# Kernel tuning notes

Measured on AMD Instinct MI355X. Metric: run time of the kernel, lower is better.

## Reference

```python
import jax, jax.numpy as jnp
import numpy as np

NUM_CLASSES = 91
BBOX_XFORM_CLIP = float(np.log(1000.0 / 16.0))
WX, WY, WW, WH = 10.0, 10.0, 5.0, 5.0  # torchvision BoxCoder weights
DETECTIONS_PER_IMG = 100


def _decode_boxes(reg, props):
    # reg: [P, 4*C], props: [P, 4] -> [P, C, 4]  (torchvision BoxCoder.decode)
    widths = props[:, 2] - props[:, 0]
    heights = props[:, 3] - props[:, 1]
    ctr_x = props[:, 0] + 0.5 * widths
    ctr_y = props[:, 1] + 0.5 * heights
    r = reg.reshape(reg.shape[0], -1, 4)
    dx = r[..., 0] / WX
    dy = r[..., 1] / WY
    dw = jnp.minimum(r[..., 2] / WW, BBOX_XFORM_CLIP)
    dh = jnp.minimum(r[..., 3] / WH, BBOX_XFORM_CLIP)
    pcx = dx * widths[:, None] + ctr_x[:, None]
    pcy = dy * heights[:, None] + ctr_y[:, None]
    pw = jnp.exp(dw) * widths[:, None]
    ph = jnp.exp(dh) * heights[:, None]
    return jnp.stack([pcx - 0.5 * pw, pcy - 0.5 * ph, pcx + 0.5 * pw, pcy + 0.5 * ph], axis=-1)


def _clip_boxes(boxes, h, w):
    x = jnp.clip(boxes[..., 0::2], 0.0, float(w))
    y = jnp.clip(boxes[..., 1::2], 0.0, float(h))
    return jnp.stack([x[..., 0], y[..., 0], x[..., 1], y[..., 1]], axis=-1)


def setup_inputs() -> dict:
    key = jax.random.key(0)
    k1, k2, k3, k4, k5 = jax.random.split(key, 5)
    B, P, C, FD = 8, 4096, NUM_CLASSES, 1024
    N = B * P
    class_logits = jax.random.normal(k1, (N, C), dtype=jnp.float32)
    box_regression = 0.5 * jax.random.normal(k2, (N, 4 * C), dtype=jnp.float32)
    # valid proposal boxes inside an 800x800 image: x1<x2, y1<y2
    xy = jax.random.uniform(k3, (N, 2), dtype=jnp.float32) * 700.0
    wh = jax.random.uniform(k4, (N, 2), dtype=jnp.float32) * 96.0 + 4.0
    proposals = jnp.concatenate([xy, xy + wh], axis=-1)
    box_features = jax.random.normal(k5, (N, FD), dtype=jnp.float32)
    return {"class_logits": class_logits, "box_regression": box_regression,
            "proposals": proposals, "box_features": box_features,
            "batch_size": B, "image_h": 800, "image_w": 800}


def reference(class_logits, box_regression, proposals, box_features, batch_size, image_h, image_w):
    B = int(batch_size)
    N = class_logits.shape[0]
    P = N // B
    lg = class_logits.reshape(B, P, NUM_CLASSES)
    rg = box_regression.reshape(B, P, 4 * NUM_CLASSES)
    pr = proposals.reshape(B, P, 4)
    ft = box_features.reshape(B, P, -1)

    def per_image(lg_i, rg_i, pr_i, ft_i):
        boxes = _decode_boxes(rg_i, pr_i)            # [P, C, 4]
        scores = jax.nn.softmax(lg_i, axis=-1)       # [P, C]
        boxes = _clip_boxes(boxes, image_h, image_w)
        boxes = boxes[:, 1:].reshape(-1, 4)          # drop background class -> [P*(C-1), 4]
        scores = scores[:, 1:].reshape(-1)
        # batched_nms with iou_threshold=1.0 never suppresses anything (IoU<=1 always),
        # so keep == indices sorted by score descending, truncated to detections_per_img.
        keep = jnp.argsort(-scores)[:DETECTIONS_PER_IMG]
        boxes = boxes / float(image_h)               # source divides by image_shape[0] only
        kept_boxes = boxes[keep]                     # [D, 4]
        feat_idx = keep // (NUM_CLASSES - 1)         # source: keep / (num_classes-1) int div
        kept_feats = ft_i[feat_idx]                  # [D, FD]
        return kept_boxes, kept_feats

    all_boxes, all_features = jax.vmap(per_image)(lg, rg, pr, ft)
    return all_boxes, all_features
```

## Files before the change

kernel.cpp:

```cpp
#include <hip/hip_runtime.h>
#include <hip/hip_bf16.h>

#define NCLS 91
#define NFG 90
#define NDET 100
#define FDIM 1024
#define CAP 4096
#define NBUK 4096
#define BBOX_CLIP 4.135166556742356f
#define K1_TPB 256
#define RPB 32
#define K2_TPB 1024

__global__ __launch_bounds__(K1_TPB) void k1_softhist(
        const float* __restrict__ logits, float* __restrict__ rowoff,
        unsigned* __restrict__ maxk, unsigned* __restrict__ ghist,
        int P, int bpi) {
    __shared__ unsigned hist[NBUK];
    for (int b = threadIdx.x; b < NBUK; b += K1_TPB) hist[b] = 0u;
    __syncthreads();
    int img = blockIdx.x / bpi;
    int blk = blockIdx.x % bpi;
    int wave = threadIdx.x >> 6, lane = threadIdx.x & 63;
    for (int it = 0; it < RPB / 4; it++) {
        int rl = blk * RPB + wave * (RPB / 4) + it;
        if (rl >= P) break;
        long long row = (long long)img * P + rl;
        const float* r = logits + row * NCLS;
        float l1 = r[lane];
        float l2 = (lane < NCLS - 64) ? r[64 + lane] : -INFINITY;
        float m = fmaxf(l1, l2);
        #pragma unroll
        for (int o = 32; o; o >>= 1) m = fmaxf(m, __shfl_xor(m, o));
        float e = expf(l1 - m) + ((lane < NCLS - 64) ? expf(l2 - m) : 0.0f);
        #pragma unroll
        for (int o = 32; o; o >>= 1) e += __shfl_xor(e, o);
        float off = m + logf(e);
        unsigned ka = (lane >= 1) ? __float_as_uint(expf(l1 - off)) : 0u;
        unsigned kb = (lane < NCLS - 64) ? __float_as_uint(expf(l2 - off)) : 0u;
        if (lane >= 1)        atomicAdd(&hist[ka >> 20], 1u);
        if (lane < NCLS - 64) atomicAdd(&hist[kb >> 20], 1u);
        unsigned km = ka > kb ? ka : kb;
        #pragma unroll
        for (int o = 32; o; o >>= 1) { unsigned t = __shfl_xor(km, o); km = km > t ? km : t; }
        if (lane == 0) { rowoff[row] = off; maxk[row] = km; }
    }
    __syncthreads();
    unsigned* gh = ghist + (size_t)img * NBUK;
    for (int b = threadIdx.x; b < NBUK; b += K1_TPB) {
        unsigned c = hist[b];
        if (c) atomicAdd(&gh[b], c);
    }
}

__global__ __launch_bounds__(K2_TPB) void k2_select(
        const float* __restrict__ logits, const float* __restrict__ reg,
        const float* __restrict__ props, const float* __restrict__ feats,
        const int* __restrict__ pH, const int* __restrict__ pW,
        const float* __restrict__ rowoff, const unsigned* __restrict__ maxk,
        const unsigned* __restrict__ ghist,
        float* __restrict__ outBoxes, float* __restrict__ outFeats, int P) {
    __shared__ unsigned long long cand[CAP];
    __shared__ unsigned hot[CAP];
    __shared__ unsigned tpart[256];
    __shared__ unsigned tsuf[257];
    __shared__ unsigned keepR[NDET];
    __shared__ unsigned sh_lb, sh_nhot, sh_ncand, sh_base;

    const int img = blockIdx.x;
    const int tid = threadIdx.x;
    const unsigned* gh = ghist + (size_t)img * NBUK;

    if (tid == 0) { sh_nhot = 0; sh_ncand = 0; sh_lb = 0; }

    unsigned local[16];
    if (tid < 256) {
        unsigned mn = 0xFFFFFFFFu;
        #pragma unroll
        for (int i = 0; i < 16; i++) { local[i] = gh[tid * 16 + i]; mn = mn < local[i] ? mn : local[i]; }
        tpart[tid] = mn;
    }
    __syncthreads();
    if (tid == 0) {
        unsigned mn = 0xFFFFFFFFu;
        for (int t = 0; t < 256; t++) mn = mn < tpart[t] ? mn : tpart[t];
        sh_base = mn;
    }
    __syncthreads();
    unsigned base = sh_base;

    if (tid < 256) {
        unsigned s = 0;
        #pragma unroll
        for (int i = 0; i < 16; i++) { local[i] -= base; s += local[i]; }
        tpart[tid] = s;
    }
    __syncthreads();
    if (tid == 0) {
        unsigned run = 0; tsuf[256] = 0;
        for (int t = 255; t >= 0; t--) { run += tpart[t]; tsuf[t] = run; }
    }
    __syncthreads();
    if (tid < 256) {
        unsigned run = tsuf[tid + 1];
        #pragma unroll
        for (int i = 15; i >= 0; i--) {
            unsigned prev = run; run += local[i];
            if (run >= NDET && prev < NDET) sh_lb = ((unsigned)(tid * 16 + i)) << 20;
        }
    }
    __syncthreads();
    const unsigned lb = sh_lb;

    const unsigned* mk = maxk + (size_t)img * P;
    for (int r = tid; r < P; r += K2_TPB)
        if (mk[r] >= lb) hot[atomicAdd(&sh_nhot, 1u)] = (unsigned)r;
    __syncthreads();
    const int nhot = (int)sh_nhot;

    const int wave = tid >> 6, lane = tid & 63;
    for (int i = wave; i < nhot; i += K2_TPB / 64) {
        int rl = (int)hot[i];
        long long row = (long long)img * P + rl;
        float off = rowoff[row];
        const float* r = logits + row * NCLS;
        float l1 = r[lane];
        float l2 = (lane < NCLS - 64) ? r[64 + lane] : -INFINITY;
        if (lane >= 1) {
            unsigned k = __float_as_uint(expf(l1 - off));
            if (k >= lb) {
                unsigned pos = atomicAdd(&sh_ncand, 1u);
                if (pos < CAP)
                    cand[pos] = ((unsigned long long)k << 32) |
                                (unsigned)(0xFFFFFFFFu - (unsigned)(rl * NFG + lane - 1));
            }
        }
        if (lane < NCLS - 64) {
            unsigned k = __float_as_uint(expf(l2 - off));
            if (k >= lb) {
                unsigned pos = atomicAdd(&sh_ncand, 1u);
                if (pos < CAP)
                    cand[pos] = ((unsigned long long)k << 32) |
                                (unsigned)(0xFFFFFFFFu - (unsigned)(rl * NFG + 63 + lane));
            }
        }
    }
    __syncthreads();
    unsigned cnt = sh_ncand; if (cnt > CAP) cnt = CAP;

    int n = 128; while (n < (int)cnt) n <<= 1;
    for (int i = tid; i < n; i += K2_TPB) if (i >= (int)cnt) cand[i] = 0ULL;
    __syncthreads();
    for (int k = 2; k <= n; k <<= 1) {
        for (int j = k >> 1; j > 0; j >>= 1) {
            for (int i = tid; i < n; i += K2_TPB) {
                int ixj = i ^ j;
                if (ixj > i) {
                    bool up = ((i & k) == 0);
                    unsigned long long a = cand[i], b = cand[ixj];
                    if ((a > b) == up) { cand[i] = b; cand[ixj] = a; }
                }
            }
            __syncthreads();
        }
    }

    if (tid < NDET) {
        unsigned long long key = cand[n - 1 - tid];
        unsigned e = 0xFFFFFFFFu - (unsigned)(key & 0xFFFFFFFFull);
        int pr = e / NFG, cm = e - pr * NFG, c = cm + 1;
        long long rw = (long long)img * P + pr;
        float x1 = props[rw * 4 + 0], y1 = props[rw * 4 + 1];
        float x2 = props[rw * 4 + 2], y2 = props[rw * 4 + 3];
        float w = x2 - x1, hgt = y2 - y1;
        float cx = x1 + 0.5f * w, cy = y1 + 0.5f * hgt;
        const float* rr = reg + rw * (4 * NCLS) + 4 * c;
        float dx = rr[0] / 10.0f, dy = rr[1] / 10.0f;
        float dw = fminf(rr[2] / 5.0f, BBOX_CLIP);
        float dh = fminf(rr[3] / 5.0f, BBOX_CLIP);
        float pcx = dx * w + cx, pcy = dy * hgt + cy;
        float pw_ = expf(dw) * w, ph_ = expf(dh) * hgt;
        float bx1 = pcx - 0.5f * pw_, by1 = pcy - 0.5f * ph_;
        float bx2 = pcx + 0.5f * pw_, by2 = pcy + 0.5f * ph_;
        float W = (float)(*pW), H = (float)(*pH);
        bx1 = fminf(fmaxf(bx1, 0.0f), W);
        bx2 = fminf(fmaxf(bx2, 0.0f), W);
        by1 = fminf(fmaxf(by1, 0.0f), H);
        by2 = fminf(fmaxf(by2, 0.0f), H);
        int o = (img * NDET + tid) * 4;
        outBoxes[o + 0] = bx1 / H;
        outBoxes[o + 1] = by1 / H;
        outBoxes[o + 2] = bx2 / H;
        outBoxes[o + 3] = by2 / H;
        keepR[tid] = (unsigned)rw;
    }
    __syncthreads();

    int g = tid >> 8, l = tid & 255;
    for (int r0 = 0; r0 < (NDET + 3) / 4; r0++) {
        int d = r0 * 4 + g;
        if (d < NDET) {
            long long rw = keepR[d];
            const float4* src = (const float4*)(feats + rw * FDIM);
            float4* dst = (float4*)(outFeats + ((long long)img * NDET + d) * FDIM);
            dst[l] = src[l];
        }
    }
}

extern "C" void kernel_launch(void* const* d_in, const int* in_sizes, int n_in,
                              void* d_out, int out_size, void* d_ws, size_t ws_size,
                              hipStream_t stream) {
    const float* logits = (const float*)d_in[0];
    const float* reg    = (const float*)d_in[1];
    const float* props  = (const float*)d_in[2];
    const float* feats  = (const float*)d_in[3];
    const int*   pH     = (const int*)d_in[5];
    const int*   pW     = (const int*)d_in[6];

    int N = in_sizes[0] / NCLS;
    int B = out_size / (NDET * (4 + FDIM));
    int P = N / B;
    int bpi = (P + RPB - 1) / RPB;

    char* ws = (char*)d_ws;
    float*    rowoff = (float*)ws;
    unsigned* maxk   = (unsigned*)(rowoff + N);
    unsigned* ghist  = (unsigned*)(maxk + N);

    float* outBoxes = (float*)d_out;
    float* outFeats = outBoxes + (size_t)B * NDET * 4;

    k1_softhist<<<B * bpi, K1_TPB, 0, stream>>>(logits, rowoff, maxk, ghist, P, bpi);
    k2_select<<<B, K2_TPB, 0, stream>>>(logits, reg, props, feats, pH, pW,
                                        rowoff, maxk, ghist, outBoxes, outFeats, P);
}
```

Measured before the change: 242.0 us.

## Build per-image histogram from row max keys and split feature gather into kernel

The first kernel no longer builds a per-score shared histogram or does global atomics. It only computes each row's log-sum-exp offset and maximum score key. The selection kernel now builds a histogram of the per-row maxima (P entries) in shared memory to find the threshold bucket, which removes the per-class atomics and the global histogram. The feature copy moves out of the 8-block selection kernel into a separate kernel with one block per detection, so it runs across many CUs. The trade-off is an extra launch and a coarser threshold from row maxima, which may admit more hot rows.

```diff
diff --git a/kernel.cpp b/kernel.cpp
--- a/kernel.cpp
+++ b/kernel.cpp
@@ -7,25 +7,20 @@
 #define FDIM 1024
 #define CAP 4096
 #define NBUK 4096
+#define PMAX 4096
 #define BBOX_CLIP 4.135166556742356f
 #define K1_TPB 256
 #define RPB 32
 #define K2_TPB 1024
 
-__global__ __launch_bounds__(K1_TPB) void k1_softhist(
+__global__ __launch_bounds__(K1_TPB) void k1_soft(
         const float* __restrict__ logits, float* __restrict__ rowoff,
-        unsigned* __restrict__ maxk, unsigned* __restrict__ ghist,
-        int P, int bpi) {
-    __shared__ unsigned hist[NBUK];
-    for (int b = threadIdx.x; b < NBUK; b += K1_TPB) hist[b] = 0u;
-    __syncthreads();
-    int img = blockIdx.x / bpi;
-    int blk = blockIdx.x % bpi;
+        unsigned* __restrict__ maxk, int N) {
     int wave = threadIdx.x >> 6, lane = threadIdx.x & 63;
+    int rowbase = blockIdx.x * RPB + wave * (RPB / 4);
     for (int it = 0; it < RPB / 4; it++) {
-        int rl = blk * RPB + wave * (RPB / 4) + it;
-        if (rl >= P) break;
-        long long row = (long long)img * P + rl;
+        long long row = rowbase + it;
+        if (row >= N) return;
         const float* r = logits + row * NCLS;
         float l1 = r[lane];
         float l2 = (lane < NCLS - 64) ? r[64 + lane] : -INFINITY;
@@ -38,61 +33,43 @@
         float off = m + logf(e);
         unsigned ka = (lane >= 1) ? __float_as_uint(expf(l1 - off)) : 0u;
         unsigned kb = (lane < NCLS - 64) ? __float_as_uint(expf(l2 - off)) : 0u;
-        if (lane >= 1)        atomicAdd(&hist[ka >> 20], 1u);
-        if (lane < NCLS - 64) atomicAdd(&hist[kb >> 20], 1u);
         unsigned km = ka > kb ? ka : kb;
         #pragma unroll
         for (int o = 32; o; o >>= 1) { unsigned t = __shfl_xor(km, o); km = km > t ? km : t; }
         if (lane == 0) { rowoff[row] = off; maxk[row] = km; }
     }
-    __syncthreads();
-    unsigned* gh = ghist + (size_t)img * NBUK;
-    for (int b = threadIdx.x; b < NBUK; b += K1_TPB) {
-        unsigned c = hist[b];
-        if (c) atomicAdd(&gh[b], c);
-    }
 }
 
 __global__ __launch_bounds__(K2_TPB) void k2_select(
         const float* __restrict__ logits, const float* __restrict__ reg,
-        const float* __restrict__ props, const float* __restrict__ feats,
+        const float* __restrict__ props,
         const int* __restrict__ pH, const int* __restrict__ pW,
         const float* __restrict__ rowoff, const unsigned* __restrict__ maxk,
-        const unsigned* __restrict__ ghist,
-        float* __restrict__ outBoxes, float* __restrict__ outFeats, int P) {
+        float* __restrict__ outBoxes, unsigned* __restrict__ keepRow, int P) {
     __shared__ unsigned long long cand[CAP];
-    __shared__ unsigned hot[CAP];
+    __shared__ unsigned hist[NBUK];
+    __shared__ unsigned hot[PMAX];
     __shared__ unsigned tpart[256];
     __shared__ unsigned tsuf[257];
     __shared__ unsigned keepR[NDET];
-    __shared__ unsigned sh_lb, sh_nhot, sh_ncand, sh_base;
+    __shared__ unsigned sh_lb, sh_nhot, sh_ncand;
 
     const int img = blockIdx.x;
     const int tid = threadIdx.x;
-    const unsigned* gh = ghist + (size_t)img * NBUK;
+    const unsigned* mk = maxk + (size_t)img * P;
 
     if (tid == 0) { sh_nhot = 0; sh_ncand = 0; sh_lb = 0; }
+    for (int b = tid; b < NBUK; b += K2_TPB) hist[b] = 0u;
+    __syncthreads();
+
+    for (int r = tid; r < P; r += K2_TPB) atomicAdd(&hist[mk[r] >> 20], 1u);
+    __syncthreads();
 
     unsigned local[16];
     if (tid < 256) {
-        unsigned mn = 0xFFFFFFFFu;
-        #pragma unroll
-        for (int i = 0; i < 16; i++) { local[i] = gh[tid * 16 + i]; mn = mn < local[i] ? mn : local[i]; }
-        tpart[tid] = mn;
-    }
-    __syncthreads();
-    if (tid == 0) {
-        unsigned mn = 0xFFFFFFFFu;
-        for (int t = 0; t < 256; t++) mn = mn < tpart[t] ? mn : tpart[t];
-        sh_base = mn;
-    }
-    __syncthreads();
-    unsigned base = sh_base;
-
-    if (tid < 256) {
         unsigned s = 0;
         #pragma unroll
-        for (int i = 0; i < 16; i++) { local[i] -= base; s += local[i]; }
+        for (int i = 0; i < 16; i++) { local[i] = hist[tid * 16 + i]; s += local[i]; }
         tpart[tid] = s;
     }
     __syncthreads();
@@ -112,7 +89,6 @@
     __syncthreads();
     const unsigned lb = sh_lb;
 
-    const unsigned* mk = maxk + (size_t)img * P;
     for (int r = tid; r < P; r += K2_TPB)
         if (mk[r] >= lb) hot[atomicAdd(&sh_nhot, 1u)] = (unsigned)r;
     __syncthreads();
@@ -192,20 +168,18 @@
         outBoxes[o + 1] = by1 / H;
         outBoxes[o + 2] = bx2 / H;
         outBoxes[o + 3] = by2 / H;
-        keepR[tid] = (unsigned)rw;
-    }
-    __syncthreads();
-
-    int g = tid >> 8, l = tid & 255;
-    for (int r0 = 0; r0 < (NDET + 3) / 4; r0++) {
-        int d = r0 * 4 + g;
-        if (d < NDET) {
-            long long rw = keepR[d];
-            const float4* src = (const float4*)(feats + rw * FDIM);
-            float4* dst = (float4*)(outFeats + ((long long)img * NDET + d) * FDIM);
-            dst[l] = src[l];
-        }
-    }
+        keepRow[img * NDET + tid] = (unsigned)rw;
+    }
+}
+
+__global__ __launch_bounds__(256) void k3_feats(
+        const float* __restrict__ feats, const unsigned* __restrict__ keepRow,
+        float* __restrict__ outF) {
+    int det = blockIdx.x;
+    long long r = keepRow[det];
+    const float4* src = (const float4*)(feats + r * FDIM);
+    float4* dst = (float4*)(outF + (long long)det * FDIM);
+    dst[threadIdx.x] = src[threadIdx.x];
 }
 
 extern "C" void kernel_launch(void* const* d_in, const int* in_sizes, int n_in,
@@ -221,17 +195,17 @@
     int N = in_sizes[0] / NCLS;
     int B = out_size / (NDET * (4 + FDIM));
     int P = N / B;
-    int bpi = (P + RPB - 1) / RPB;
 
     char* ws = (char*)d_ws;
-    float*    rowoff = (float*)ws;
-    unsigned* maxk   = (unsigned*)(rowoff + N);
-    unsigned* ghist  = (unsigned*)(maxk + N);
+    float*    rowoff  = (float*)ws;
+    unsigned* maxk    = (unsigned*)(rowoff + N);
+    unsigned* keepRow = (unsigned*)(maxk + N);
 
     float* outBoxes = (float*)d_out;
     float* outFeats = outBoxes + (size_t)B * NDET * 4;
 
-    k1_softhist<<<B * bpi, K1_TPB, 0, stream>>>(logits, rowoff, maxk, ghist, P, bpi);
-    k2_select<<<B, K2_TPB, 0, stream>>>(logits, reg, props, feats, pH, pW,
-                                        rowoff, maxk, ghist, outBoxes, outFeats, P);
-}
+    k1_soft<<<(N + RPB - 1) / RPB, K1_TPB, 0, stream>>>(logits, rowoff, maxk, N);
+    k2_select<<<B, K2_TPB, 0, stream>>>(logits, reg, props, pH, pW,
+                                        rowoff, maxk, outBoxes, keepRow, P);
+    k3_feats<<<B * NDET, 256, 0, stream>>>(feats, keepRow, outFeats);
+}
```

New measurement: 228.2 us. -5.7%, faster.
